# Kernel tuning notes

Hardware: AMD Instinct MI355X
Metric: run time of the kernel (lower is better)

The kernel has to match this reference:

```python
import jax, jax.numpy as jnp
import numpy as np

EMBED_DIM = 1024
N_HEADS = 16
HEAD_DIM = EMBED_DIM // N_HEADS


def setup_inputs() -> dict:
    key = jax.random.key(0)
    k1, k2, k3 = jax.random.split(key, 3)
    B, T, C = 2, 2048, EMBED_DIM
    x = jax.random.normal(k1, (B, T, C), dtype=jnp.float32)
    # nn.Linear-style init scale
    s = 1.0 / np.sqrt(C)
    Wqkv = jax.random.normal(k2, (C, 3 * C), dtype=jnp.float32) * s
    bqkv = jnp.zeros((3 * C,), dtype=jnp.float32)
    Wout = jax.random.normal(k3, (C, C), dtype=jnp.float32) * s
    bout = jnp.zeros((C,), dtype=jnp.float32)
    return {"x": x, "Wqkv": Wqkv, "bqkv": bqkv, "Wout": Wout, "bout": bout}


def reference(x, Wqkv, bqkv, Wout, bout):
    B, T, C = x.shape
    H, D = N_HEADS, HEAD_DIM
    qkv = x @ Wqkv + bqkv  # [B,T,3C]
    q, k, v = jnp.split(qkv, 3, axis=-1)
    # [B,T,C] -> [B,H,T,D]
    q = q.reshape(B, T, H, D).transpose(0, 2, 1, 3)
    k = k.reshape(B, T, H, D).transpose(0, 2, 1, 3)
    v = v.reshape(B, T, H, D).transpose(0, 2, 1, 3)
    scale = 1.0 / np.sqrt(D)
    scores = jnp.einsum("bhqd,bhkd->bhqk", q, k) * scale  # [B,H,T,T]
    causal = jnp.tril(jnp.ones((T, T), dtype=bool))  # True where allowed
    scores = jnp.where(causal, scores, jnp.finfo(scores.dtype).min)
    attn = jax.nn.softmax(scores, axis=-1)
    out = jnp.einsum("bhqk,bhkd->bhqd", attn, v)  # [B,H,T,D]
    out = out.transpose(0, 2, 1, 3).reshape(B, T, C)
    return out @ Wout + bout
```

## Files before the change

kernel.cpp:

```cpp
#include <hip/hip_runtime.h>
#include <hip/hip_bf16.h>
#include <stdint.h>

#define EMBED 1024
#define NH 16
#define HD 64
#define BATCH 2
#define SEQ 2048
#define MTOK (BATCH*SEQ)

using bf8 = __attribute__((ext_vector_type(8))) short;
using f4  = __attribute__((ext_vector_type(4))) float;
using f16v = __attribute__((ext_vector_type(16))) float;
using u16x4 = __attribute__((ext_vector_type(4))) unsigned short;

union U4 { uint32_t u[4]; bf8 v; };

__device__ __forceinline__ uint32_t pk_bf16(float a, float b) {
  __hip_bfloat162 h = __float22bfloat162_rn(float2{a, b});
  union { __hip_bfloat162 h; uint32_t u; } c; c.h = h; return c.u;
}
__device__ __forceinline__ unsigned short bfbits(float f) {
  __hip_bfloat16 h = __float2bfloat16(f);
  union { __hip_bfloat16 h; unsigned short u; } c; c.h = h; return c.u;
}
__device__ __forceinline__ float bf2f(unsigned short u) {
  union { uint32_t u; float f; } c; c.u = (uint32_t)u << 16; return c.f;
}
__device__ __forceinline__ float fexp2(float x) {
#if __has_builtin(__builtin_amdgcn_exp2f)
  return __builtin_amdgcn_exp2f(x);
#else
  return exp2f(x);
#endif
}
__device__ __forceinline__ float frcp(float x) {
#if __has_builtin(__builtin_amdgcn_rcpf)
  return __builtin_amdgcn_rcpf(x);
#else
  return 1.f / x;
#endif
}

__device__ __forceinline__ void gl2lds16(const void* g, void* l) {
  __builtin_amdgcn_global_load_lds(
      (const __attribute__((address_space(1))) void*)g,
      (__attribute__((address_space(3))) void*)l, 16, 0, 0);
}

__global__ __launch_bounds__(256) void prep(const float* __restrict__ x,
                                            unsigned short* __restrict__ xb,
                                            const float* __restrict__ Wqkv,
                                            unsigned short* __restrict__ wqkvT,
                                            const float* __restrict__ Wout,
                                            unsigned short* __restrict__ woutT) {
  __shared__ float tl[64][65];
  int blk = blockIdx.x;
  if (blk < 4096) {
    int i = (blk * 256 + threadIdx.x) * 4;
    float4 v = *(const float4*)(x + i);
    uint2 o;
    o.x = pk_bf16(v.x, v.y);
    o.y = pk_bf16(v.z, v.w);
    *(uint2*)(xb + i) = o;
    return;
  }
  const float* W; unsigned short* Wt; int K, N, bx, by;
  if (blk < 4096 + 768) {
    int j = blk - 4096; W = Wqkv; Wt = wqkvT; K = 1024; N = 3072;
    bx = j % 48; by = j / 48;
  } else {
    int j = blk - 4096 - 768; W = Wout; Wt = woutT; K = 1024; N = 1024;
    bx = j % 16; by = j / 16;
  }
  int k0 = by * 64, n0 = bx * 64;
  int tr = threadIdx.x >> 6, tc = threadIdx.x & 63;
#pragma unroll
  for (int i = 0; i < 16; i++) {
    int r = tr + i * 4;
    tl[r][tc] = W[(size_t)(k0 + r) * N + n0 + tc];
  }
  __syncthreads();
#pragma unroll
  for (int i = 0; i < 16; i++) {
    int r = tr + i * 4;
    Wt[(size_t)(n0 + r) * K + k0 + tc] = bfbits(tl[tc][r]);
  }
}

template<int BN, int MODE>
__global__ __launch_bounds__(256) void gemm_bt(const unsigned short* __restrict__ A,
                                               const unsigned short* __restrict__ Bt,
                                               const float* __restrict__ bias,
                                               unsigned short* __restrict__ Oq,
                                               unsigned short* __restrict__ Ov,
                                               float* __restrict__ Of,
                                               int M, int N, int K) {
  constexpr int MT = (BN == 128) ? 4 : 2;
  const int tid = threadIdx.x;
  const int w = tid >> 6, lane = tid & 63;
  const int wm = (BN == 128) ? (w >> 1) : w;
  const int wn = (BN == 128) ? (w & 1) : 0;
  const int m0 = blockIdx.y * 128, n0 = blockIdx.x * BN;

  __shared__ char smem[16384 + BN * 128];
  char* Al = smem;
  char* Bl = smem + 16384;

  f4 acc[MT][4] = {};

  for (int k0 = 0; k0 < K; k0 += 64) {
    __syncthreads();
#pragma unroll
    for (int i = 0; i < 4; i++) {
      int row = w * 8 + i * 32 + (lane >> 3);
      int col = ((lane & 7) * 8) ^ ((row & 7) << 3);
      gl2lds16(A + (size_t)(m0 + row) * K + k0 + col, Al + (w * 8 + i * 32) * 128);
    }
#pragma unroll
    for (int i = 0; i < BN / 32; i++) {
      int row = w * 8 + i * 32 + (lane >> 3);
      int col = ((lane & 7) * 8) ^ ((row & 7) << 3);
      gl2lds16(Bt + (size_t)(n0 + row) * K + k0 + col, Bl + (w * 8 + i * 32) * 128);
    }
    __syncthreads();
#pragma unroll
    for (int ks = 0; ks < 2; ks++) {
      bf8 af[MT], bfr[4];
#pragma unroll
      for (int mt = 0; mt < MT; mt++) {
        int rr = wm * (MT * 16) + mt * 16 + (lane & 15);
        af[mt] = *(const bf8*)(Al + rr * 128 + ((ks * 64 + (lane >> 4) * 16) ^ ((rr & 7) << 4)));
      }
#pragma unroll
      for (int nt = 0; nt < 4; nt++) {
        int rr = wn * 64 + nt * 16 + (lane & 15);
        bfr[nt] = *(const bf8*)(Bl + rr * 128 + ((ks * 64 + (lane >> 4) * 16) ^ ((rr & 7) << 4)));
      }
#pragma unroll
      for (int mt = 0; mt < MT; mt++)
#pragma unroll
        for (int nt = 0; nt < 4; nt++)
          acc[mt][nt] = __builtin_amdgcn_mfma_f32_16x16x32_bf16(af[mt], bfr[nt], acc[mt][nt], 0, 0, 0);
    }
  }

  if (MODE == 0) {
#pragma unroll
    for (int nt = 0; nt < 4; nt++) {
      int n = n0 + wn * 64 + nt * 16 + (lane & 15);
      float bv = bias[n];
      int region = n >> 10, c = n & 1023, h = c >> 6, d = c & 63;
      float sc = (region == 0) ? 0.180336880f : 1.0f;
#pragma unroll
      for (int mt = 0; mt < MT; mt++) {
#pragma unroll
        for (int r = 0; r < 4; r++) {
          int m = m0 + wm * (MT * 16) + mt * 16 + (lane >> 4) * 4 + r;
          int b = m >> 11, t = m & 2047;
          unsigned short val = bfbits((acc[mt][nt][r] + bv) * sc);
          if (region < 2) {
            size_t off = ((((size_t)region * 2 + b) * 16 + h) * 2048 + t) * 64 + d;
            Oq[off] = val;
          } else {
            size_t off = (((size_t)b * 16 + h) * 64 + d) * 2048 + t;
            Ov[off] = val;
          }
        }
      }
    }
  } else {
#pragma unroll
    for (int mt = 0; mt < MT; mt++) {
#pragma unroll
      for (int r = 0; r < 4; r++) {
        int m = m0 + wm * (MT * 16) + mt * 16 + (lane >> 4) * 4 + r;
#pragma unroll
        for (int nt = 0; nt < 4; nt++) {
          int n = n0 + wn * 64 + nt * 16 + (lane & 15);
          Of[(size_t)m * N + n] = acc[mt][nt][r] + bias[n];
        }
      }
    }
  }
}

__global__ __launch_bounds__(256) void attn11(const unsigned short* __restrict__ Qb,
                                              const unsigned short* __restrict__ Kb,
                                              const unsigned short* __restrict__ Vtb,
                                              unsigned short* __restrict__ Ob,
                                              unsigned short* __restrict__ partO,
                                              float* __restrict__ Lbuf) {
  static const signed char QTs[32] = {15,15,14,14,13,13,12,12,11,11,10,10,9,8,7,6,5,15,4,9,14,3,8,13,2,7,12,1,6,11,0,5};
  static const signed char TSs[32] = {0,11,0,11,0,11,0,11,0,11,0,11,0,0,0,0,0,22,0,11,22,0,11,22,0,11,22,0,11,22,0,11};
  static const signed char PS[32]  = {0,1,2,3,4,5,6,7,8,9,10,11,12,13,14,15,16,17,-1,18,19,-1,20,21,-1,22,23,-1,24,25,-1,26};
  const int idx = blockIdx.x;
  const int s = idx >> 5, bh = idx & 31;
  const int qt = QTs[s], ts = TSs[s];
  const int ntot = 2 * qt + 2;
  const int te = min(ts + 11, ntot);
  const int slot = PS[s];

  const int tid = threadIdx.x;
  const int w = tid >> 6, lane = tid & 63;
  const int hi = lane >> 5, q32 = lane & 31;

  __shared__ char smem[32768];

  const unsigned short* Qg  = Qb  + (size_t)bh * SEQ * HD;
  const unsigned short* Kg  = Kb  + (size_t)bh * SEQ * HD;
  const unsigned short* Vtg = Vtb + (size_t)bh * SEQ * HD;

  const int qbw  = qt * 128 + w * 32;
  const int qrow = qbw + q32;

  bf8 qf[4];
#pragma unroll
  for (int kc = 0; kc < 4; kc++)
    qf[kc] = *(const bf8*)(Qg + (size_t)qrow * HD + kc * 16 + hi * 8);

  U4 ones;
#pragma unroll
  for (int i = 0; i < 4; i++) ones.u[i] = 0x3F803F80u;

  f16v acc0 = {}, acc1 = {}, accl = {};

  auto STAGE = [&](int buf, int t) {
    int kv0 = t * 64;
#pragma unroll
    for (int i = 0; i < 2; i++) {
      int c = i * 4 + w;
      int row = c * 8 + (lane >> 3);
      int col = ((lane & 7) * 8) ^ ((row & 7) << 3);
      gl2lds16(Kg + (size_t)(kv0 + row) * HD + col,    smem + buf * 8192 + c * 1024);
      gl2lds16(Vtg + (size_t)row * SEQ + kv0 + col,    smem + 16384 + buf * 8192 + c * 1024);
    }
  };

  const int nt_loc = te - ts;
  STAGE(0, ts);
  if (nt_loc > 1) STAGE(1, ts + 1);

  for (int tl = 0; tl < nt_loc; tl++) {
    const int t = ts + tl;
    const int kv0 = t * 64;

    if (tl + 1 < nt_loc) {
      asm volatile("s_waitcnt vmcnt(4)" ::: "memory");
    } else {
      asm volatile("s_waitcnt vmcnt(0)" ::: "memory");
    }
    __builtin_amdgcn_s_barrier();

    if (kv0 <= qbw + 31) {
      const char* kl = smem + (tl & 1) * 8192;
      const char* vl = smem + 16384 + (tl & 1) * 8192;
      const bool hi_vis = (kv0 + 32 <= qbw + 31);

      f16v s0 = {}, s1 = {};
      __builtin_amdgcn_s_setprio(1);
#pragma unroll
      for (int kc = 0; kc < 4; kc++) {
        int r0 = q32;
        bf8 k0 = *(const bf8*)(kl + r0 * 128 + ((kc * 32 + hi * 16) ^ ((r0 & 7) << 4)));
        s0 = __builtin_amdgcn_mfma_f32_32x32x16_bf16(k0, qf[kc], s0, 0, 0, 0);
      }
      if (hi_vis) {
#pragma unroll
        for (int kc = 0; kc < 4; kc++) {
          int r1 = 32 + q32;
          bf8 k1 = *(const bf8*)(kl + r1 * 128 + ((kc * 32 + hi * 16) ^ ((r1 & 7) << 4)));
          s1 = __builtin_amdgcn_mfma_f32_32x32x16_bf16(k1, qf[kc], s1, 0, 0, 0);
        }
      }
      __builtin_amdgcn_s_setprio(0);

      if (kv0 + 63 > qbw) {
#pragma unroll
        for (int r = 0; r < 16; r++) {
          int key = kv0 + (r & 3) + 8 * (r >> 2) + 4 * hi;
          if (key > qrow)      s0[r] = -1e30f;
          if (key + 32 > qrow) s1[r] = -1e30f;
        }
      }

      uint32_t u[16];
#pragma unroll
      for (int m8 = 0; m8 < 8; m8++) {
        float pa = fexp2(s0[2 * m8]), pb = fexp2(s0[2 * m8 + 1]);
        u[m8] = pk_bf16(pa, pb);
      }
      if (hi_vis) {
#pragma unroll
        for (int m8 = 0; m8 < 8; m8++) {
          float pc = fexp2(s1[2 * m8]), pd = fexp2(s1[2 * m8 + 1]);
          u[8 + m8] = pk_bf16(pc, pd);
        }
      }

      __builtin_amdgcn_s_setprio(1);
      const int ncc = hi_vis ? 4 : 2;
      for (int kcc = 0; kcc < ncc; kcc++) {
        const int base = (kcc >> 1) * 8 + (kcc & 1) * 4;
        uint32_t a0 = u[base + 0], a2 = u[base + 2];
        uint32_t a1 = u[base + 1], a3 = u[base + 3];
        asm("v_permlane32_swap_b32 %0, %1" : "+v"(a0), "+v"(a2));
        asm("v_permlane32_swap_b32 %0, %1" : "+v"(a1), "+v"(a3));
        U4 f; f.u[0] = a0; f.u[1] = a1; f.u[2] = a2; f.u[3] = a3;
        int r0 = q32, r1 = 32 + q32;
        bf8 v0 = *(const bf8*)(vl + r0 * 128 + ((kcc * 32 + hi * 16) ^ ((r0 & 7) << 4)));
        bf8 v1 = *(const bf8*)(vl + r1 * 128 + ((kcc * 32 + hi * 16) ^ ((r1 & 7) << 4)));
        acc0 = __builtin_amdgcn_mfma_f32_32x32x16_bf16(f.v, v0, acc0, 0, 0, 0);
        acc1 = __builtin_amdgcn_mfma_f32_32x32x16_bf16(f.v, v1, acc1, 0, 0, 0);
        accl = __builtin_amdgcn_mfma_f32_32x32x16_bf16(f.v, ones.v, accl, 0, 0, 0);
      }
      __builtin_amdgcn_s_setprio(0);
    }

    __builtin_amdgcn_s_barrier();
    if (tl + 2 < nt_loc) STAGE(tl & 1, t + 2);
  }

  if (slot < 0) {
    int b = bh >> 4, h = bh & 15;
    unsigned short* Og = Ob + (size_t)b * SEQ * EMBED;
#pragma unroll
    for (int r = 0; r < 16; r++) {
      int ql_ = (r & 3) + 8 * (r >> 2) + 4 * hi;
      float linv = frcp(accl[r]);
      size_t rowoff = (size_t)(qbw + ql_) * EMBED + h * 64;
      Og[rowoff + q32]      = bfbits(acc0[r] * linv);
      Og[rowoff + 32 + q32] = bfbits(acc1[r] * linv);
    }
  } else {
    int pidx = slot * 32 + bh;
    unsigned short* P0 = partO + (size_t)pidx * 8192;
#pragma unroll
    for (int r = 0; r < 16; r++) {
      int ql_ = (r & 3) + 8 * (r >> 2) + 4 * hi;
      int rowl = w * 32 + ql_;
      P0[rowl * 64 + q32]      = bfbits(acc0[r]);
      P0[rowl * 64 + 32 + q32] = bfbits(acc1[r]);
    }
    if (q32 == 0) {
#pragma unroll
      for (int r = 0; r < 16; r++) {
        int ql_ = (r & 3) + 8 * (r >> 2) + 4 * hi;
        Lbuf[pidx * 128 + w * 32 + ql_] = accl[r];
      }
    }
  }
}

__global__ __launch_bounds__(256) void attn_combine(const unsigned short* __restrict__ partO,
                                                    const float* __restrict__ Lbuf,
                                                    unsigned short* __restrict__ Ob) {
  static const signed char NSg[11] = {2,2,2,2,2,2,3,3,3,3,3};
  static const signed char SL[11][3] = {
    {16,26,0},{15,24,0},{14,22,0},{13,20,0},{12,18,0},{10,11,0},
    {8,9,25},{6,7,23},{4,5,21},{2,3,19},{0,1,17}};
  int pair = blockIdx.x;
  int qi = pair >> 5, bh = pair & 31;
  int qt = 5 + qi;
  int ns = NSg[qi];
  int b = bh >> 4, h = bh & 15;
#pragma unroll
  for (int rr = 0; rr < 2; rr++) {
    int row = rr * 64 + (threadIdx.x >> 2);
    int d0 = (threadIdx.x & 3) * 16;
    float lsum = 0.f;
    float acc[16] = {};
    for (int sg = 0; sg < ns; sg++) {
      int pidx = (int)SL[qi][sg] * 32 + bh;
      lsum += Lbuf[pidx * 128 + row];
      const unsigned short* O0 = partO + (size_t)pidx * 8192 + row * 64 + d0;
#pragma unroll
      for (int v = 0; v < 4; v++) {
        u16x4 a = *(const u16x4*)(O0 + v * 4);
#pragma unroll
        for (int e = 0; e < 4; e++) acc[v * 4 + e] += bf2f(a[e]);
      }
    }
    float linv = 1.f / lsum;
    unsigned short* out = Ob + ((size_t)b * SEQ + qt * 128 + row) * EMBED + h * 64 + d0;
    u16x4 res[4];
#pragma unroll
    for (int v = 0; v < 4; v++) {
#pragma unroll
      for (int e = 0; e < 4; e++) res[v][e] = bfbits(acc[v * 4 + e] * linv);
    }
    *(u16x4*)(out)      = res[0];
    *(u16x4*)(out + 4)  = res[1];
    *(u16x4*)(out + 8)  = res[2];
    *(u16x4*)(out + 12) = res[3];
  }
}

extern "C" void kernel_launch(void* const* d_in, const int* in_sizes, int n_in,
                              void* d_out, int out_size, void* d_ws, size_t ws_size,
                              hipStream_t stream) {
  const float* x    = (const float*)d_in[0];
  const float* Wqkv = (const float*)d_in[1];
  const float* bqkv = (const float*)d_in[2];
  const float* Wout = (const float*)d_in[3];
  const float* bout = (const float*)d_in[4];
  float* out = (float*)d_out;

  char* ws = (char*)d_ws;
  unsigned short* xb    = (unsigned short*)ws;
  unsigned short* wqkvT = (unsigned short*)(ws + (size_t)8 * 1048576);
  unsigned short* partO = (unsigned short*)ws;
  float*          lbuf  = (float*)(ws + 14155776);
  unsigned short* woutT = (unsigned short*)(ws + (size_t)14 * 1048576);
  unsigned short* qk    = (unsigned short*)(ws + (size_t)16 * 1048576);
  unsigned short* vT    = (unsigned short*)(ws + (size_t)32 * 1048576);
  unsigned short* obuf  = (unsigned short*)(ws + (size_t)40 * 1048576);

  prep<<<dim3(4096 + 768 + 256), 256, 0, stream>>>(x, xb, Wqkv, wqkvT, Wout, woutT);

  gemm_bt<128, 0><<<dim3(24, 32), 256, 0, stream>>>(xb, wqkvT, bqkv, qk, vT, nullptr,
                                                    MTOK, 3 * EMBED, EMBED);

  const unsigned short* Qb = qk;
  const unsigned short* Kb = qk + (size_t)BATCH * NH * SEQ * HD;
  attn11<<<dim3(32 * 32), 256, 0, stream>>>(Qb, Kb, vT, obuf, partO, lbuf);
  attn_combine<<<dim3(11 * 32), 256, 0, stream>>>(partO, lbuf, obuf);

  gemm_bt<64, 1><<<dim3(16, 32), 256, 0, stream>>>(obuf, woutT, bout, nullptr, nullptr, out,
                                                   MTOK, EMBED, EMBED);
}
```

Baseline: 116.6 us.

## Double-buffer GEMM LDS loads and use 128x64 tiles for QKV projection

Rewrites the bf16 GEMM as a two-stage software pipeline. Global-to-LDS loads for tile k+2 are issued while tile k is computed, with vmcnt waits and s_barrier replacing the two __syncthreads per step, and s_setprio raised around the MFMA block. The QKV projection switches from 128x128 to 128x64 tiles, doubling the grid and halving the accumulators per wave, and the V-transpose epilogue now writes four packed bf16 values per store instead of scalars. The aim is to hide global load latency and raise occupancy; the cost is more LDS per block and more blocks re-reading A.

```diff
diff --git a/kernel.cpp b/kernel.cpp
--- a/kernel.cpp
+++ b/kernel.cpp
@@ -88,7 +88,7 @@
   }
 }
 
-template<int BN, int MODE>
+template<int MODE>
 __global__ __launch_bounds__(256) void gemm_bt(const unsigned short* __restrict__ A,
                                                const unsigned short* __restrict__ Bt,
                                                const float* __restrict__ bias,
@@ -96,88 +96,118 @@
                                                unsigned short* __restrict__ Ov,
                                                float* __restrict__ Of,
                                                int M, int N, int K) {
-  constexpr int MT = (BN == 128) ? 4 : 2;
   const int tid = threadIdx.x;
   const int w = tid >> 6, lane = tid & 63;
-  const int wm = (BN == 128) ? (w >> 1) : w;
-  const int wn = (BN == 128) ? (w & 1) : 0;
-  const int m0 = blockIdx.y * 128, n0 = blockIdx.x * BN;
-
-  __shared__ char smem[16384 + BN * 128];
-  char* Al = smem;
-  char* Bl = smem + 16384;
-
-  f4 acc[MT][4] = {};
-
-  for (int k0 = 0; k0 < K; k0 += 64) {
-    __syncthreads();
+  const int m0 = blockIdx.y * 128, n0 = blockIdx.x * 64;
+
+  __shared__ char smem[49152];
+  f4 acc[2][4] = {};
+
+  auto STAGE = [&](int buf, int kk) {
+    int k0 = kk * 64;
 #pragma unroll
     for (int i = 0; i < 4; i++) {
-      int row = w * 8 + i * 32 + (lane >> 3);
+      int c = i * 4 + w;
+      int row = c * 8 + (lane >> 3);
       int col = ((lane & 7) * 8) ^ ((row & 7) << 3);
-      gl2lds16(A + (size_t)(m0 + row) * K + k0 + col, Al + (w * 8 + i * 32) * 128);
-    }
-#pragma unroll
-    for (int i = 0; i < BN / 32; i++) {
-      int row = w * 8 + i * 32 + (lane >> 3);
+      gl2lds16(A + (size_t)(m0 + row) * K + k0 + col, smem + buf * 16384 + c * 1024);
+    }
+#pragma unroll
+    for (int i = 0; i < 2; i++) {
+      int c = i * 4 + w;
+      int row = c * 8 + (lane >> 3);
       int col = ((lane & 7) * 8) ^ ((row & 7) << 3);
-      gl2lds16(Bt + (size_t)(n0 + row) * K + k0 + col, Bl + (w * 8 + i * 32) * 128);
-    }
-    __syncthreads();
+      gl2lds16(Bt + (size_t)(n0 + row) * K + k0 + col, smem + 32768 + buf * 8192 + c * 1024);
+    }
+  };
+
+  const int nk = K / 64;
+  STAGE(0, 0);
+  STAGE(1, 1);
+
+  for (int kk = 0; kk < nk; kk++) {
+    if (kk + 1 < nk) {
+      asm volatile("s_waitcnt vmcnt(6)" ::: "memory");
+    } else {
+      asm volatile("s_waitcnt vmcnt(0)" ::: "memory");
+    }
+    __builtin_amdgcn_s_barrier();
+
+    const char* Al = smem + (kk & 1) * 16384;
+    const char* Bl = smem + 32768 + (kk & 1) * 8192;
+    __builtin_amdgcn_s_setprio(1);
 #pragma unroll
     for (int ks = 0; ks < 2; ks++) {
-      bf8 af[MT], bfr[4];
-#pragma unroll
-      for (int mt = 0; mt < MT; mt++) {
-        int rr = wm * (MT * 16) + mt * 16 + (lane & 15);
+      bf8 af[2], bfr[4];
+#pragma unroll
+      for (int mt = 0; mt < 2; mt++) {
+        int rr = w * 32 + mt * 16 + (lane & 15);
         af[mt] = *(const bf8*)(Al + rr * 128 + ((ks * 64 + (lane >> 4) * 16) ^ ((rr & 7) << 4)));
       }
 #pragma unroll
       for (int nt = 0; nt < 4; nt++) {
-        int rr = wn * 64 + nt * 16 + (lane & 15);
+        int rr = nt * 16 + (lane & 15);
         bfr[nt] = *(const bf8*)(Bl + rr * 128 + ((ks * 64 + (lane >> 4) * 16) ^ ((rr & 7) << 4)));
       }
 #pragma unroll
-      for (int mt = 0; mt < MT; mt++)
+      for (int mt = 0; mt < 2; mt++)
 #pragma unroll
         for (int nt = 0; nt < 4; nt++)
           acc[mt][nt] = __builtin_amdgcn_mfma_f32_16x16x32_bf16(af[mt], bfr[nt], acc[mt][nt], 0, 0, 0);
     }
+    __builtin_amdgcn_s_setprio(0);
+
+    __builtin_amdgcn_s_barrier();
+    if (kk + 2 < nk) STAGE(kk & 1, kk + 2);
   }
 
   if (MODE == 0) {
-#pragma unroll
-    for (int nt = 0; nt < 4; nt++) {
-      int n = n0 + wn * 64 + nt * 16 + (lane & 15);
-      float bv = bias[n];
-      int region = n >> 10, c = n & 1023, h = c >> 6, d = c & 63;
+    const int region = n0 >> 10;
+    if (region < 2) {
       float sc = (region == 0) ? 0.180336880f : 1.0f;
 #pragma unroll
-      for (int mt = 0; mt < MT; mt++) {
-#pragma unroll
-        for (int r = 0; r < 4; r++) {
-          int m = m0 + wm * (MT * 16) + mt * 16 + (lane >> 4) * 4 + r;
+      for (int nt = 0; nt < 4; nt++) {
+        int n = n0 + nt * 16 + (lane & 15);
+        float bv = bias[n];
+        int c = n & 1023, h = c >> 6, d = c & 63;
+#pragma unroll
+        for (int mt = 0; mt < 2; mt++) {
+#pragma unroll
+          for (int r = 0; r < 4; r++) {
+            int m = m0 + w * 32 + mt * 16 + (lane >> 4) * 4 + r;
+            int b = m >> 11, t = m & 2047;
+            size_t off = ((((size_t)region * 2 + b) * 16 + h) * 2048 + t) * 64 + d;
+            Oq[off] = bfbits((acc[mt][nt][r] + bv) * sc);
+          }
+        }
+      }
+    } else {
+#pragma unroll
+      for (int nt = 0; nt < 4; nt++) {
+        int n = n0 + nt * 16 + (lane & 15);
+        float bv = bias[n];
+        int c = n & 1023, h = c >> 6, d = c & 63;
+#pragma unroll
+        for (int mt = 0; mt < 2; mt++) {
+          int m = m0 + w * 32 + mt * 16 + (lane >> 4) * 4;
           int b = m >> 11, t = m & 2047;
-          unsigned short val = bfbits((acc[mt][nt][r] + bv) * sc);
-          if (region < 2) {
-            size_t off = ((((size_t)region * 2 + b) * 16 + h) * 2048 + t) * 64 + d;
-            Oq[off] = val;
-          } else {
-            size_t off = (((size_t)b * 16 + h) * 64 + d) * 2048 + t;
-            Ov[off] = val;
-          }
+          size_t off = (((size_t)b * 16 + h) * 64 + d) * 2048 + t;
+          u16x4 pk4;
+#pragma unroll
+          for (int r = 0; r < 4; r++) pk4[r] = bfbits(acc[mt][nt][r] + bv);
+          *(u16x4*)(Ov + off) = pk4;
         }
       }
     }
   } else {
 #pragma unroll
-    for (int mt = 0; mt < MT; mt++) {
+    for (int mt = 0; mt < 2; mt++) {
 #pragma unroll
       for (int r = 0; r < 4; r++) {
-        int m = m0 + wm * (MT * 16) + mt * 16 + (lane >> 4) * 4 + r;
+        int m = m0 + w * 32 + mt * 16 + (lane >> 4) * 4 + r;
 #pragma unroll
         for (int nt = 0; nt < 4; nt++) {
-          int n = n0 + wn * 64 + nt * 16 + (lane & 15);
+          int n = n0 + nt * 16 + (lane & 15);
           Of[(size_t)m * N + n] = acc[mt][nt][r] + bias[n];
         }
       }
@@ -418,14 +448,14 @@
 
   prep<<<dim3(4096 + 768 + 256), 256, 0, stream>>>(x, xb, Wqkv, wqkvT, Wout, woutT);
 
-  gemm_bt<128, 0><<<dim3(24, 32), 256, 0, stream>>>(xb, wqkvT, bqkv, qk, vT, nullptr,
-                                                    MTOK, 3 * EMBED, EMBED);
+  gemm_bt<0><<<dim3(48, 32), 256, 0, stream>>>(xb, wqkvT, bqkv, qk, vT, nullptr,
+                                               MTOK, 3 * EMBED, EMBED);
 
   const unsigned short* Qb = qk;
   const unsigned short* Kb = qk + (size_t)BATCH * NH * SEQ * HD;
   attn11<<<dim3(32 * 32), 256, 0, stream>>>(Qb, Kb, vT, obuf, partO, lbuf);
   attn_combine<<<dim3(11 * 32), 256, 0, stream>>>(partO, lbuf, obuf);
 
-  gemm_bt<64, 1><<<dim3(16, 32), 256, 0, stream>>>(obuf, woutT, bout, nullptr, nullptr, out,
-                                                   MTOK, EMBED, EMBED);
-}
+  gemm_bt<1><<<dim3(16, 32), 256, 0, stream>>>(obuf, woutT, bout, nullptr, nullptr, out,
+                                               MTOK, EMBED, EMBED);
+}
```

Measured after the change: 109.0 us. 1.07x faster.
